# Kernel tuning notes

Hardware: AMD Instinct MI355X
Metric: run time of the kernel (lower is better)

Reference implementation:

```python
import jax, jax.numpy as jnp
import numpy as np

N_STEP = 8
DILATION = 1


def setup_inputs() -> dict:
    key = jax.random.key(0)
    k1, k2 = jax.random.split(key)
    B, C, T, V = 32, 128, 64, 25
    z = jax.random.normal(k1, (B, C, T, V), dtype=jnp.float32)
    W = jax.random.normal(k2, (C, C), dtype=jnp.float32) * 0.02  # channel-mixing ode weight
    b = jnp.zeros((C,), dtype=jnp.float32)
    return {"z": z, "W": W, "b": b}


def reference(z, W, b):
    # z: (B, C, T, V). ode_func acts per-frame on (C, V): linear over channels + tanh.
    B, C, T, V = z.shape

    def ode_func(x):
        # equivalent to applying the C->C linear on the '(b t) c v' layout
        return jnp.tanh(jnp.einsum('bctv,dc->bdtv', x, W) + b[None, :, None, None])

    t_idx = jnp.arange(T)
    z_shift_lst = [z]
    z_lst = [z]
    cur = z
    for i in range(1, N_STEP + 1):
        cur = cur + ode_func(cur)                      # Euler step
        shift = i * DILATION
        # gather with index (arange(T) - shift) % T  ==  circular roll by +shift along T
        rolled = jnp.roll(cur, shift, axis=2)
        mask = (t_idx >= shift)[None, None, :, None]   # zero the first shift frames
        z_shift_lst.append(jnp.where(mask, rolled, jnp.zeros((), cur.dtype)))
        z_lst.append(cur)
    z_shift = jnp.concatenate(z_shift_lst, axis=0)     # ((n_step+1)*B, C, T, V)
    z_cls = jnp.concatenate(z_lst, axis=0)             # ((n_step+1)*B, C, T, V)
    return (z_shift, z_cls)
```

## Files before the change

kernel.cpp:

```cpp
#include <hip/hip_runtime.h>

#define CC     128
#define TT     64
#define VV     25
#define BB     32
#define PP     (TT * VV)
#define CHUNK  (BB * CC * PP)
#define NSTEP  8
#define PTILE  32
#define NPT    (PP / PTILE)

typedef __attribute__((ext_vector_type(8))) __bf16 bf16x8;
typedef __attribute__((ext_vector_type(4))) float  f32x4;

__device__ __forceinline__ float fast_tanh(float x) {
    float e = __expf(2.0f * x);
    return 1.0f - 2.0f * __builtin_amdgcn_rcpf(e + 1.0f);
}

__device__ __forceinline__ void bf16_split(float y, unsigned short& h, unsigned short& lo) {
    unsigned int bits = __float_as_uint(y);
    h = (unsigned short)(bits >> 16);
    float r = y - __uint_as_float(bits & 0xffff0000u);
    lo = (unsigned short)(__float_as_uint(r) >> 16);
}

__device__ __forceinline__ int xb_off(int p, int c) {
    return (p * 256 + c * 2) ^ ((p & 7) << 4) ^ ((p & 8) << 3);
}

__device__ __forceinline__ void lds_barrier() {
    asm volatile("s_waitcnt lgkmcnt(0)" ::: "memory");
    __builtin_amdgcn_sched_barrier(0);
    __builtin_amdgcn_s_barrier();
    __builtin_amdgcn_sched_barrier(0);
}

__global__ void wsplit(const float* __restrict__ W,
                       unsigned short* __restrict__ Wh, unsigned short* __restrict__ Wl) {
    int idx = blockIdx.x * 256 + threadIdx.x;
    if (idx < CC * CC) {
        unsigned short h, lo;
        bf16_split(W[idx], h, lo);
        Wh[idx] = h;
        Wl[idx] = lo;
    }
}

__global__ __launch_bounds__(256, 4) void euler_fused(
    const float* __restrict__ z, const unsigned short* __restrict__ Wh,
    const unsigned short* __restrict__ Wl, const float* __restrict__ bias,
    float* __restrict__ out)
{
    __shared__ unsigned short XH[2][PTILE * CC];
    __shared__ unsigned short XL[2][PTILE * CC];

    const int b   = blockIdx.y;
    const int p0  = blockIdx.x * PTILE;
    const int tid = threadIdx.x;
    const int w   = tid >> 6;
    const int lr  = tid & 15;
    const int lh  = (tid >> 4) & 3;

    bf16x8 wh[2][4], wl[2][4];
    #pragma unroll
    for (int dt = 0; dt < 2; ++dt) {
        const int d = (2 * w + dt) * 16 + lr;
        #pragma unroll
        for (int ks = 0; ks < 4; ++ks) {
            const int cb = ks * 32 + lh * 8;
            wh[dt][ks] = *(const bf16x8*)(Wh + d * CC + cb);
            wl[dt][ks] = *(const bf16x8*)(Wl + d * CC + cb);
        }
    }

    float bv[2];
    #pragma unroll
    for (int dt = 0; dt < 2; ++dt) bv[dt] = bias[(2 * w + dt) * 16 + lr];

    const float* zb = z + (size_t)b * CC * PP + p0;
    #pragma unroll
    for (int it = 0; it < 4; ++it) {
        int slot = it * 256 + tid;
        int c  = slot >> 3;
        int po = (slot & 7) * 4;
        float4 v = *(const float4*)(zb + (size_t)c * PP + po);
        size_t o = (size_t)(b * CC + c) * PP + p0 + po;
        *(float4*)(out + o)                     = v;
        *(float4*)(out + (size_t)9 * CHUNK + o) = v;
        float vv[4] = {v.x, v.y, v.z, v.w};
        #pragma unroll
        for (int e = 0; e < 4; ++e) {
            unsigned short h, lo;
            bf16_split(vv[e], h, lo);
            int off = xb_off(po + e, c);
            *(unsigned short*)((char*)XH[0] + off) = h;
            *(unsigned short*)((char*)XL[0] + off) = lo;
        }
    }

    f32x4 st[2][2];
    #pragma unroll
    for (int pt = 0; pt < 2; ++pt)
        #pragma unroll
        for (int dt = 0; dt < 2; ++dt) {
            const int d = (2 * w + dt) * 16 + lr;
            st[pt][dt] = *(const f32x4*)(z + (size_t)(b * CC + d) * PP + p0 + pt * 16 + lh * 4);
        }

    lds_barrier();

    const int swz = ((lr & 7) << 4) ^ ((lr & 8) << 3);

    for (int i = 1; i <= NSTEP; ++i) {
        const char* xh = (const char*)XH[(i - 1) & 1];
        const char* xl = (const char*)XL[(i - 1) & 1];

        f32x4 acc[2][2];
        #pragma unroll
        for (int pt = 0; pt < 2; ++pt)
            #pragma unroll
            for (int dt = 0; dt < 2; ++dt)
                acc[pt][dt] = (f32x4){0.0f, 0.0f, 0.0f, 0.0f};

        #pragma unroll
        for (int ks = 0; ks < 4; ++ks) {
            const int co = ks * 64 + lh * 16;
            const int r0 = ((lr)      * 256 + co) ^ swz;
            const int r1 = ((16 + lr) * 256 + co) ^ swz;
            bf16x8 a0h = *(const bf16x8*)(xh + r0);
            bf16x8 a1h = *(const bf16x8*)(xh + r1);
            bf16x8 a0l = *(const bf16x8*)(xl + r0);
            bf16x8 a1l = *(const bf16x8*)(xl + r1);
            #pragma unroll
            for (int dt = 0; dt < 2; ++dt) {
                acc[0][dt] = __builtin_amdgcn_mfma_f32_16x16x32_bf16(a0h, wh[dt][ks], acc[0][dt], 0, 0, 0);
                acc[1][dt] = __builtin_amdgcn_mfma_f32_16x16x32_bf16(a1h, wh[dt][ks], acc[1][dt], 0, 0, 0);
                acc[0][dt] = __builtin_amdgcn_mfma_f32_16x16x32_bf16(a0l, wh[dt][ks], acc[0][dt], 0, 0, 0);
                acc[1][dt] = __builtin_amdgcn_mfma_f32_16x16x32_bf16(a1l, wh[dt][ks], acc[1][dt], 0, 0, 0);
                acc[0][dt] = __builtin_amdgcn_mfma_f32_16x16x32_bf16(a0h, wl[dt][ks], acc[0][dt], 0, 0, 0);
                acc[1][dt] = __builtin_amdgcn_mfma_f32_16x16x32_bf16(a1h, wl[dt][ks], acc[1][dt], 0, 0, 0);
            }
        }

        #pragma unroll
        for (int pt = 0; pt < 2; ++pt)
            #pragma unroll
            for (int dt = 0; dt < 2; ++dt)
                #pragma unroll
                for (int j = 0; j < 4; ++j)
                    st[pt][dt][j] += fast_tanh(acc[pt][dt][j] + bv[dt]);

        if (i < NSTEP) {
            char* yh = (char*)XH[i & 1];
            char* yl = (char*)XL[i & 1];
            #pragma unroll
            for (int pt = 0; pt < 2; ++pt)
                #pragma unroll
                for (int dt = 0; dt < 2; ++dt) {
                    const int d = (2 * w + dt) * 16 + lr;
                    #pragma unroll
                    for (int j = 0; j < 4; ++j) {
                        const int p = pt * 16 + lh * 4 + j;
                        unsigned short h, lo;
                        bf16_split(st[pt][dt][j], h, lo);
                        const int off = xb_off(p, d);
                        *(unsigned short*)(yh + off) = h;
                        *(unsigned short*)(yl + off) = lo;
                    }
                }
        }

        const size_t shiftBase = (size_t)i * CHUNK;
        const size_t clsBase   = (size_t)(9 + i) * CHUNK;
        const int s = VV * i;
        const bool fast = (p0 >= s) && (p0 + PTILE - 1 + s < PP);
        #pragma unroll
        for (int pt = 0; pt < 2; ++pt) {
            const int P0 = p0 + pt * 16 + lh * 4;
            #pragma unroll
            for (int dt = 0; dt < 2; ++dt) {
                const int d = (2 * w + dt) * 16 + lr;
                const size_t row = (size_t)(b * CC + d) * PP;
                f32x4 y = st[pt][dt];
                *(f32x4*)(out + clsBase + row + P0) = y;
                if (fast) {
                    float* dst = out + shiftBase + row + P0 + s;
                    dst[0] = y[0]; dst[1] = y[1]; dst[2] = y[2]; dst[3] = y[3];
                } else {
                    #pragma unroll
                    for (int e = 0; e < 4; ++e) {
                        const int p = P0 + e, q = p + s;
                        if (q < PP) out[shiftBase + row + q] = y[e];
                        if (p < s)  out[shiftBase + row + p] = 0.0f;
                    }
                }
            }
        }

        if (i < NSTEP) lds_barrier();
    }
}

extern "C" void kernel_launch(void* const* d_in, const int* in_sizes, int n_in,
                              void* d_out, int out_size, void* d_ws, size_t ws_size,
                              hipStream_t stream) {
    const float* z    = (const float*)d_in[0];
    const float* W    = (const float*)d_in[1];
    const float* bias = (const float*)d_in[2];
    float* out = (float*)d_out;
    unsigned short* Wh = (unsigned short*)d_ws;
    unsigned short* Wl = Wh + CC * CC;

    hipLaunchKernelGGL(wsplit, dim3((CC * CC + 255) / 256), dim3(256), 0, stream, W, Wh, Wl);
    hipLaunchKernelGGL(euler_fused, dim3(NPT, BB), dim3(256), 0, stream, z, Wh, Wl, bias, out);
}
```

Measured before the change: 688.9 us.

## Double pixel tile, fuse weight split, use nontemporal stores, unroll steps

Doubles the pixel tile per block to 64, so each block reuses its register-held weights across twice the work. The separate weight-splitting kernel is folded into the main kernel, which removes one launch. All output writes become nontemporal stores to reduce cache pollution on this write-bound kernel, and shifted stores use paired 8-byte writes when alignment allows. The step loop is fully unrolled. In exchange, register and LDS use roughly double, the launch_bounds occupancy hint is dropped, and the grid has half as many blocks.

Result: slower. 869.7 us (+26.3%).

```diff
diff --git a/kernel.cpp b/kernel.cpp
--- a/kernel.cpp
+++ b/kernel.cpp
@@ -7,11 +7,12 @@
 #define PP     (TT * VV)
 #define CHUNK  (BB * CC * PP)
 #define NSTEP  8
-#define PTILE  32
+#define PTILE  64
 #define NPT    (PP / PTILE)
 
 typedef __attribute__((ext_vector_type(8))) __bf16 bf16x8;
 typedef __attribute__((ext_vector_type(4))) float  f32x4;
+typedef __attribute__((ext_vector_type(2))) float  f32x2;
 
 __device__ __forceinline__ float fast_tanh(float x) {
     float e = __expf(2.0f * x);
@@ -36,21 +37,9 @@
     __builtin_amdgcn_sched_barrier(0);
 }
 
-__global__ void wsplit(const float* __restrict__ W,
-                       unsigned short* __restrict__ Wh, unsigned short* __restrict__ Wl) {
-    int idx = blockIdx.x * 256 + threadIdx.x;
-    if (idx < CC * CC) {
-        unsigned short h, lo;
-        bf16_split(W[idx], h, lo);
-        Wh[idx] = h;
-        Wl[idx] = lo;
-    }
-}
-
-__global__ __launch_bounds__(256, 4) void euler_fused(
-    const float* __restrict__ z, const unsigned short* __restrict__ Wh,
-    const unsigned short* __restrict__ Wl, const float* __restrict__ bias,
-    float* __restrict__ out)
+__global__ __launch_bounds__(256) void euler_fused(
+    const float* __restrict__ z, const float* __restrict__ W,
+    const float* __restrict__ bias, float* __restrict__ out)
 {
     __shared__ unsigned short XH[2][PTILE * CC];
     __shared__ unsigned short XL[2][PTILE * CC];
@@ -62,15 +51,23 @@
     const int lr  = tid & 15;
     const int lh  = (tid >> 4) & 3;
 
+    union BF8 { bf16x8 v; unsigned short u[8]; };
     bf16x8 wh[2][4], wl[2][4];
     #pragma unroll
     for (int dt = 0; dt < 2; ++dt) {
         const int d = (2 * w + dt) * 16 + lr;
         #pragma unroll
         for (int ks = 0; ks < 4; ++ks) {
-            const int cb = ks * 32 + lh * 8;
-            wh[dt][ks] = *(const bf16x8*)(Wh + d * CC + cb);
-            wl[dt][ks] = *(const bf16x8*)(Wl + d * CC + cb);
+            const float* wp = W + d * CC + ks * 32 + lh * 8;
+            f32x4 f0 = *(const f32x4*)wp;
+            f32x4 f1 = *(const f32x4*)(wp + 4);
+            BF8 th, tl;
+            #pragma unroll
+            for (int e = 0; e < 4; ++e) bf16_split(f0[e], th.u[e],     tl.u[e]);
+            #pragma unroll
+            for (int e = 0; e < 4; ++e) bf16_split(f1[e], th.u[4 + e], tl.u[4 + e]);
+            wh[dt][ks] = th.v;
+            wl[dt][ks] = tl.v;
         }
     }
 
@@ -80,28 +77,27 @@
 
     const float* zb = z + (size_t)b * CC * PP + p0;
     #pragma unroll
-    for (int it = 0; it < 4; ++it) {
+    for (int it = 0; it < 8; ++it) {
         int slot = it * 256 + tid;
-        int c  = slot >> 3;
-        int po = (slot & 7) * 4;
-        float4 v = *(const float4*)(zb + (size_t)c * PP + po);
+        int c  = slot >> 4;
+        int po = (slot & 15) * 4;
+        f32x4 v = *(const f32x4*)(zb + (size_t)c * PP + po);
         size_t o = (size_t)(b * CC + c) * PP + p0 + po;
-        *(float4*)(out + o)                     = v;
-        *(float4*)(out + (size_t)9 * CHUNK + o) = v;
-        float vv[4] = {v.x, v.y, v.z, v.w};
+        __builtin_nontemporal_store(v, (f32x4*)(out + o));
+        __builtin_nontemporal_store(v, (f32x4*)(out + (size_t)9 * CHUNK + o));
         #pragma unroll
         for (int e = 0; e < 4; ++e) {
             unsigned short h, lo;
-            bf16_split(vv[e], h, lo);
+            bf16_split(v[e], h, lo);
             int off = xb_off(po + e, c);
             *(unsigned short*)((char*)XH[0] + off) = h;
             *(unsigned short*)((char*)XL[0] + off) = lo;
         }
     }
 
-    f32x4 st[2][2];
-    #pragma unroll
-    for (int pt = 0; pt < 2; ++pt)
+    f32x4 st[4][2];
+    #pragma unroll
+    for (int pt = 0; pt < 4; ++pt)
         #pragma unroll
         for (int dt = 0; dt < 2; ++dt) {
             const int d = (2 * w + dt) * 16 + lr;
@@ -112,13 +108,14 @@
 
     const int swz = ((lr & 7) << 4) ^ ((lr & 8) << 3);
 
+    #pragma unroll
     for (int i = 1; i <= NSTEP; ++i) {
         const char* xh = (const char*)XH[(i - 1) & 1];
         const char* xl = (const char*)XL[(i - 1) & 1];
 
-        f32x4 acc[2][2];
-        #pragma unroll
-        for (int pt = 0; pt < 2; ++pt)
+        f32x4 acc[4][2];
+        #pragma unroll
+        for (int pt = 0; pt < 4; ++pt)
             #pragma unroll
             for (int dt = 0; dt < 2; ++dt)
                 acc[pt][dt] = (f32x4){0.0f, 0.0f, 0.0f, 0.0f};
@@ -126,25 +123,25 @@
         #pragma unroll
         for (int ks = 0; ks < 4; ++ks) {
             const int co = ks * 64 + lh * 16;
-            const int r0 = ((lr)      * 256 + co) ^ swz;
-            const int r1 = ((16 + lr) * 256 + co) ^ swz;
-            bf16x8 a0h = *(const bf16x8*)(xh + r0);
-            bf16x8 a1h = *(const bf16x8*)(xh + r1);
-            bf16x8 a0l = *(const bf16x8*)(xl + r0);
-            bf16x8 a1l = *(const bf16x8*)(xl + r1);
-            #pragma unroll
-            for (int dt = 0; dt < 2; ++dt) {
-                acc[0][dt] = __builtin_amdgcn_mfma_f32_16x16x32_bf16(a0h, wh[dt][ks], acc[0][dt], 0, 0, 0);
-                acc[1][dt] = __builtin_amdgcn_mfma_f32_16x16x32_bf16(a1h, wh[dt][ks], acc[1][dt], 0, 0, 0);
-                acc[0][dt] = __builtin_amdgcn_mfma_f32_16x16x32_bf16(a0l, wh[dt][ks], acc[0][dt], 0, 0, 0);
-                acc[1][dt] = __builtin_amdgcn_mfma_f32_16x16x32_bf16(a1l, wh[dt][ks], acc[1][dt], 0, 0, 0);
-                acc[0][dt] = __builtin_amdgcn_mfma_f32_16x16x32_bf16(a0h, wl[dt][ks], acc[0][dt], 0, 0, 0);
-                acc[1][dt] = __builtin_amdgcn_mfma_f32_16x16x32_bf16(a1h, wl[dt][ks], acc[1][dt], 0, 0, 0);
+            bf16x8 ah[4], al[4];
+            #pragma unroll
+            for (int pt = 0; pt < 4; ++pt) {
+                const int ro = ((pt * 16 + lr) * 256 + co) ^ swz;
+                ah[pt] = *(const bf16x8*)(xh + ro);
+                al[pt] = *(const bf16x8*)(xl + ro);
             }
-        }
-
-        #pragma unroll
-        for (int pt = 0; pt < 2; ++pt)
+            #pragma unroll
+            for (int pt = 0; pt < 4; ++pt)
+                #pragma unroll
+                for (int dt = 0; dt < 2; ++dt) {
+                    acc[pt][dt] = __builtin_amdgcn_mfma_f32_16x16x32_bf16(ah[pt], wh[dt][ks], acc[pt][dt], 0, 0, 0);
+                    acc[pt][dt] = __builtin_amdgcn_mfma_f32_16x16x32_bf16(al[pt], wh[dt][ks], acc[pt][dt], 0, 0, 0);
+                    acc[pt][dt] = __builtin_amdgcn_mfma_f32_16x16x32_bf16(ah[pt], wl[dt][ks], acc[pt][dt], 0, 0, 0);
+                }
+        }
+
+        #pragma unroll
+        for (int pt = 0; pt < 4; ++pt)
             #pragma unroll
             for (int dt = 0; dt < 2; ++dt)
                 #pragma unroll
@@ -155,7 +152,7 @@
             char* yh = (char*)XH[i & 1];
             char* yl = (char*)XL[i & 1];
             #pragma unroll
-            for (int pt = 0; pt < 2; ++pt)
+            for (int pt = 0; pt < 4; ++pt)
                 #pragma unroll
                 for (int dt = 0; dt < 2; ++dt) {
                     const int d = (2 * w + dt) * 16 + lr;
@@ -176,23 +173,32 @@
         const int s = VV * i;
         const bool fast = (p0 >= s) && (p0 + PTILE - 1 + s < PP);
         #pragma unroll
-        for (int pt = 0; pt < 2; ++pt) {
+        for (int pt = 0; pt < 4; ++pt) {
             const int P0 = p0 + pt * 16 + lh * 4;
             #pragma unroll
             for (int dt = 0; dt < 2; ++dt) {
                 const int d = (2 * w + dt) * 16 + lr;
                 const size_t row = (size_t)(b * CC + d) * PP;
                 f32x4 y = st[pt][dt];
-                *(f32x4*)(out + clsBase + row + P0) = y;
+                __builtin_nontemporal_store(y, (f32x4*)(out + clsBase + row + P0));
                 if (fast) {
                     float* dst = out + shiftBase + row + P0 + s;
-                    dst[0] = y[0]; dst[1] = y[1]; dst[2] = y[2]; dst[3] = y[3];
+                    if ((i & 1) == 0) {
+                        f32x2 y01 = {y[0], y[1]}, y23 = {y[2], y[3]};
+                        __builtin_nontemporal_store(y01, (f32x2*)(dst));
+                        __builtin_nontemporal_store(y23, (f32x2*)(dst + 2));
+                    } else {
+                        __builtin_nontemporal_store(y[0], dst);
+                        __builtin_nontemporal_store(y[1], dst + 1);
+                        __builtin_nontemporal_store(y[2], dst + 2);
+                        __builtin_nontemporal_store(y[3], dst + 3);
+                    }
                 } else {
                     #pragma unroll
                     for (int e = 0; e < 4; ++e) {
                         const int p = P0 + e, q = p + s;
-                        if (q < PP) out[shiftBase + row + q] = y[e];
-                        if (p < s)  out[shiftBase + row + p] = 0.0f;
+                        if (q < PP) __builtin_nontemporal_store(y[e], out + shiftBase + row + q);
+                        if (p < s)  __builtin_nontemporal_store(0.0f, out + shiftBase + row + p);
                     }
                 }
             }
@@ -209,9 +215,6 @@
     const float* W    = (const float*)d_in[1];
     const float* bias = (const float*)d_in[2];
     float* out = (float*)d_out;
-    unsigned short* Wh = (unsigned short*)d_ws;
-    unsigned short* Wl = Wh + CC * CC;
-
-    hipLaunchKernelGGL(wsplit, dim3((CC * CC + 255) / 256), dim3(256), 0, stream, W, Wh, Wl);
-    hipLaunchKernelGGL(euler_fused, dim3(NPT, BB), dim3(256), 0, stream, z, Wh, Wl, bias, out);
-}
+
+    hipLaunchKernelGGL(euler_fused, dim3(NPT, BB), dim3(256), 0, stream, z, W, bias, out);
+}
```
